# Kernel optimization log

Measured on AMD Instinct MI355X. Metric: run time of the kernel, lower is better.

Reference implementation:

```python
import jax, jax.numpy as jnp
import numpy as np

# --- constants mirroring init_kwargs ---
DIM = 1024
N_HEADS = 16
N_KV_HEADS = 4
HEAD_DIM = DIM // N_HEADS          # 64
REP = N_HEADS // N_KV_HEADS        # 4
ROPE_THETA = 10000.0
WINDOW = 512
N_GLOBAL = 64
EPS = 1e-6


def setup_inputs() -> dict:
    key = jax.random.key(0)
    ks = jax.random.split(key, 7)
    B, L = 2, 2048
    x = jax.random.normal(ks[0], (B, L, DIM), dtype=jnp.float32)
    s = 0.02
    wq = jax.random.normal(ks[1], (DIM, N_HEADS * HEAD_DIM), dtype=jnp.float32) * s
    wk = jax.random.normal(ks[2], (DIM, N_KV_HEADS * HEAD_DIM), dtype=jnp.float32) * s
    wv = jax.random.normal(ks[3], (DIM, N_KV_HEADS * HEAD_DIM), dtype=jnp.float32) * s
    wo = jax.random.normal(ks[4], (N_HEADS * HEAD_DIM, DIM), dtype=jnp.float32) * s
    gq = jnp.ones((HEAD_DIM,), dtype=jnp.float32) + 0.01 * jax.random.normal(ks[5], (HEAD_DIM,), dtype=jnp.float32)
    gk = jnp.ones((HEAD_DIM,), dtype=jnp.float32) + 0.01 * jax.random.normal(ks[6], (HEAD_DIM,), dtype=jnp.float32)
    return {"x": x, "wq": wq, "wk": wk, "wv": wv, "wo": wo, "gq": gq, "gk": gk}


def _rmsnorm(t, g):
    # QKNorm: RMS norm over head_dim with learnable per-dim scale
    return t * jax.lax.rsqrt(jnp.mean(t * t, axis=-1, keepdims=True) + EPS) * g


def _rope(t, cos, sin):
    # t: [B,H,L,hd]; complex RoPE over consecutive pairs (2i, 2i+1)
    t1 = t[..., 0::2]
    t2 = t[..., 1::2]
    o1 = t1 * cos - t2 * sin
    o2 = t1 * sin + t2 * cos
    return jnp.stack([o1, o2], axis=-1).reshape(t.shape)


def reference(x, wq, wk, wv, wo, gq, gk):
    B, L, D = x.shape
    q = (x @ wq).reshape(B, L, N_HEADS, HEAD_DIM)
    k = (x @ wk).reshape(B, L, N_KV_HEADS, HEAD_DIM)
    v = (x @ wv).reshape(B, L, N_KV_HEADS, HEAD_DIM)
    q = _rmsnorm(q, gq)
    k = _rmsnorm(k, gk)
    q = q.transpose(0, 2, 1, 3)  # [B,H,L,hd]
    k = k.transpose(0, 2, 1, 3)
    v = v.transpose(0, 2, 1, 3)

    # RoPE frequencies (start_pos = 0)
    inv_freq = 1.0 / (ROPE_THETA ** (jnp.arange(0, HEAD_DIM, 2, dtype=jnp.float32) / HEAD_DIM))
    ang = jnp.arange(L, dtype=jnp.float32)[:, None] * inv_freq[None, :]  # [L, hd/2]
    cos, sin = jnp.cos(ang), jnp.sin(ang)
    q = _rope(q, cos, sin)
    k = _rope(k, cos, sin)

    # GQA: repeat kv heads (repeat_interleave on head dim)
    k = jnp.repeat(k, REP, axis=1)
    v = jnp.repeat(v, REP, axis=1)

    scores = jnp.einsum("bhqd,bhkd->bhqk", q, k) / np.sqrt(HEAD_DIM).astype(np.float32)

    # sliding-window + global-token causal mask
    half = WINDOW // 2
    i = jnp.arange(L)[:, None]
    j = jnp.arange(L)[None, :]
    m = (j <= i) & ((j >= i - half) | (j < N_GLOBAL))  # [L,L] bool
    scores = jnp.where(m[None, None], scores, -jnp.inf)

    attn = jax.nn.softmax(scores.astype(jnp.float32), axis=-1).astype(scores.dtype)
    out = jnp.einsum("bhqk,bhkd->bhqd", attn, v)
    out = out.transpose(0, 2, 1, 3).reshape(B, L, N_HEADS * HEAD_DIM)
    return out @ wo
```

## Files before the change

### kernel.cpp

```cpp
#include <hip/hip_runtime.h>
#include <hip/hip_bf16.h>

typedef __bf16 bf16x8 __attribute__((ext_vector_type(8)));
typedef __bf16 bf16x4 __attribute__((ext_vector_type(4)));
typedef float  f32x4  __attribute__((ext_vector_type(4)));
typedef short  s16x4  __attribute__((ext_vector_type(4)));

__device__ __forceinline__ __bf16 to_bf16(float f) {
    __hip_bfloat16 h = __float2bfloat16(f);
    return *reinterpret_cast<__bf16*>(&h);
}

__device__ __forceinline__ f32x4 mfma32(bf16x8 a, bf16x8 b, f32x4 c) {
    return __builtin_amdgcn_mfma_f32_16x16x32_bf16(a, b, c, 0, 0, 0);
}
__device__ __forceinline__ f32x4 mfma16(bf16x4 a, bf16x4 b, f32x4 c) {
#if __has_builtin(__builtin_amdgcn_mfma_f32_16x16x16_bf16)
    return __builtin_amdgcn_mfma_f32_16x16x16_bf16(a, b, c, 0, 0, 0);
#else
    return __builtin_amdgcn_mfma_f32_16x16x16bf16_1k(
        __builtin_bit_cast(s16x4, a), __builtin_bit_cast(s16x4, b), c, 0, 0, 0);
#endif
}

__device__ __forceinline__ void gload_lds16(const __bf16* g, __bf16* l) {
    __builtin_amdgcn_global_load_lds(
        (const __attribute__((address_space(1))) void*)g,
        (__attribute__((address_space(3))) void*)l, 16, 0, 0);
}


__global__ __launch_bounds__(256) void prep_k(const float* __restrict__ wq,
                                              const float* __restrict__ wk,
                                              const float* __restrict__ wv,
                                              const float* __restrict__ wo,
                                              const float* __restrict__ x,
                                              __bf16* __restrict__ WqkvT,
                                              __bf16* __restrict__ WoT,
                                              __bf16* __restrict__ xb) {
    int b = blockIdx.x, tid = threadIdx.x;
    if (b >= 2560) {
        int i = ((b - 2560) * 256 + tid) * 8;
        f32x4 a = *(const f32x4*)(x + i);
        f32x4 c = *(const f32x4*)(x + i + 4);
        bf16x8 h;
        h[0] = to_bf16(a.x); h[1] = to_bf16(a.y); h[2] = to_bf16(a.z); h[3] = to_bf16(a.w);
        h[4] = to_bf16(c.x); h[5] = to_bf16(c.y); h[6] = to_bf16(c.z); h[7] = to_bf16(c.w);
        *(bf16x8*)(xb + i) = h;
        return;
    }
    __shared__ float tile[32][33];
    const float* src; __bf16* dst; int N, idx;
    if (b < 1024)      { src = wq; dst = WqkvT;                        N = 1024; idx = b; }
    else if (b < 1280) { src = wk; dst = WqkvT + (size_t)1024 * 1024;  N = 256;  idx = b - 1024; }
    else if (b < 1536) { src = wv; dst = WqkvT + (size_t)1280 * 1024;  N = 256;  idx = b - 1280; }
    else               { src = wo; dst = WoT;                          N = 1024; idx = b - 1536; }
    int k0 = (idx & 31) * 32, n0 = (idx >> 5) * 32;
    int tx = tid & 31, ty = tid >> 5;
#pragma unroll
    for (int r = 0; r < 4; ++r) {
        int kk = ty + r * 8;
        tile[kk][tx] = src[(size_t)(k0 + kk) * N + n0 + tx];
    }
    __syncthreads();
#pragma unroll
    for (int r = 0; r < 4; ++r) {
        int nn = ty + r * 8;
        dst[(size_t)(n0 + nn) * 1024 + k0 + tx] = to_bf16(tile[tx][nn]);
    }
}

__global__ __launch_bounds__(256) void gemmqkv_k(const __bf16* __restrict__ A,
                                                 const __bf16* __restrict__ BT,
                                                 const float* __restrict__ gq,
                                                 const float* __restrict__ gk,
                                                 __bf16* __restrict__ Qb,
                                                 __bf16* __restrict__ Kbl,
                                                 __bf16* __restrict__ Vt) {
    __shared__ __bf16 lA[128 * 32];
    __shared__ __bf16 lB[64 * 32];
    __shared__ float ssp[2][128];
    __shared__ __bf16 tv[64 * 136];
    const int K = 1024;
    int tid = threadIdx.x;
    int m0 = blockIdx.x * 128, n0 = blockIdx.y * 64;
    int head = n0 >> 6;
    int wid = tid >> 6, lane = tid & 63;
    int wm = (wid & 1) * 64, wn = (wid >> 1) * 32;
    int lm = lane & 15, qd = lane >> 4;

    f32x4 acc[4][2] = {};

    for (int k0 = 0; k0 < K; k0 += 32) {
#pragma unroll
        for (int it = 0; it < 2; ++it) {
            int c = it * 256 + tid;
            int row = c >> 2, c8 = c & 3;
            __bf16* la = lA + (it * 256 + wid * 64) * 8;
            gload_lds16(A + (size_t)(m0 + row) * K + k0 + c8 * 8, la);
        }
        {
            int row = tid >> 2, c8 = tid & 3;
            __bf16* lb = lB + (wid * 64) * 8;
            gload_lds16(BT + (size_t)(n0 + row) * K + k0 + c8 * 8, lb);
        }
        __syncthreads();

        bf16x8 af[4], bfr[2];
#pragma unroll
        for (int t = 0; t < 4; ++t)
            af[t] = *(const bf16x8*)&lA[(wm + t * 16 + lm) * 32 + qd * 8];
#pragma unroll
        for (int j = 0; j < 2; ++j)
            bfr[j] = *(const bf16x8*)&lB[(wn + j * 16 + lm) * 32 + qd * 8];
#pragma unroll
        for (int ti = 0; ti < 4; ++ti)
#pragma unroll
            for (int tj = 0; tj < 2; ++tj)
                acc[ti][tj] = mfma32(af[ti], bfr[tj], acc[ti][tj]);
        __syncthreads();
    }

    if (head < 20) {
#pragma unroll
        for (int ti = 0; ti < 4; ++ti)
#pragma unroll
            for (int r = 0; r < 4; ++r) {
                float sq = acc[ti][0][r] * acc[ti][0][r] + acc[ti][1][r] * acc[ti][1][r];
                sq += __shfl_xor(sq, 1);
                sq += __shfl_xor(sq, 2);
                sq += __shfl_xor(sq, 4);
                sq += __shfl_xor(sq, 8);
                if (lm == 0) ssp[wid >> 1][wm + ti * 16 + qd * 4 + r] = sq;
            }
        __syncthreads();

        bool isq = head < 16;
#pragma unroll
        for (int ti = 0; ti < 4; ++ti)
#pragma unroll
            for (int r = 0; r < 4; ++r) {
                int row = wm + ti * 16 + qd * 4 + r;
                int t = m0 + row;
                int pos = t & 2047, bb = t >> 11;
                float ss = ssp[0][row] + ssp[1][row];
                float scale = rsqrtf(ss * (1.0f / 64.0f) + 1e-6f);
#pragma unroll
                for (int tj = 0; tj < 2; ++tj) {
                    int col = wn + tj * 16 + lm;
                    float g = isq ? gq[col] : gk[col];
                    float v = acc[ti][tj][r] * scale * g;
                    float ex = (float)(2 * (col >> 1)) * (1.0f / 64.0f);
                    float invf = expf(-ex * 9.210340371976184f);
                    float ang = (float)pos * invf;
                    float c = cosf(ang), s = sinf(ang);
                    float pv = __shfl_xor(v, 1);
                    float outv = (col & 1) ? (pv * s + v * c) : (v * c - pv * s);
                    if (isq) {
                        int kvh = head >> 2, h4 = head & 3;
                        size_t off = (((((size_t)bb * 4 + kvh) * 128 + (pos >> 4)) * 4 + h4) * 16
                                      + (pos & 15)) * 64 + col;
                        Qb[off] = to_bf16(outv * 0.125f);
                    } else {
                        int kvg = head - 16;
                        Kbl[(((size_t)bb * 4 + kvg) * 2048 + pos) * 64 + col] = to_bf16(outv);
                    }
                }
            }
    } else {
#pragma unroll
        for (int ti = 0; ti < 4; ++ti)
#pragma unroll
            for (int tj = 0; tj < 2; ++tj)
#pragma unroll
                for (int r = 0; r < 4; ++r) {
                    int row = wm + ti * 16 + qd * 4 + r;
                    int col = wn + tj * 16 + lm;
                    tv[col * 136 + row] = to_bf16(acc[ti][tj][r]);
                }
        __syncthreads();
        int bb = m0 >> 11, kvg = head - 20;
        size_t gg = (size_t)bb * 4 + kvg;
        int pos0 = m0 & 2047;
#pragma unroll
        for (int p = 0; p < 4; ++p) {
            int d = p * 16 + (tid >> 4);
            int tok = (tid & 15) * 8;
            bf16x8 vvv = *(const bf16x8*)&tv[d * 136 + tok];
            *(bf16x8*)(Vt + (gg * 64 + d) * 2048 + pos0 + tok) = vvv;
        }
    }
}

__global__ __launch_bounds__(256) void gemm_bf16_k(const __bf16* __restrict__ A,
                                                   const __bf16* __restrict__ BT,
                                                   float* __restrict__ C,
                                                   int K, int N) {
    __shared__ __bf16 lA[128 * 32];
    __shared__ __bf16 lB[64 * 32];
    int tid = threadIdx.x;
    int m0 = blockIdx.x * 128, n0 = blockIdx.y * 64;
    int wid = tid >> 6, lane = tid & 63;
    int wm = (wid & 1) * 64, wn = (wid >> 1) * 32;
    int lm = lane & 15, qd = lane >> 4;

    f32x4 acc[4][2] = {};

    for (int k0 = 0; k0 < K; k0 += 32) {
#pragma unroll
        for (int it = 0; it < 2; ++it) {
            int c = it * 256 + tid;
            int row = c >> 2, c8 = c & 3;
            __bf16* la = lA + (it * 256 + wid * 64) * 8;
            gload_lds16(A + (size_t)(m0 + row) * K + k0 + c8 * 8, la);
        }
        {
            int row = tid >> 2, c8 = tid & 3;
            __bf16* lb = lB + (wid * 64) * 8;
            gload_lds16(BT + (size_t)(n0 + row) * K + k0 + c8 * 8, lb);
        }
        __syncthreads();

        bf16x8 af[4], bfr[2];
#pragma unroll
        for (int t = 0; t < 4; ++t)
            af[t] = *(const bf16x8*)&lA[(wm + t * 16 + lm) * 32 + qd * 8];
#pragma unroll
        for (int j = 0; j < 2; ++j)
            bfr[j] = *(const bf16x8*)&lB[(wn + j * 16 + lm) * 32 + qd * 8];
#pragma unroll
        for (int ti = 0; ti < 4; ++ti)
#pragma unroll
            for (int tj = 0; tj < 2; ++tj)
                acc[ti][tj] = mfma32(af[ti], bfr[tj], acc[ti][tj]);
        __syncthreads();
    }

#pragma unroll
    for (int ti = 0; ti < 4; ++ti)
#pragma unroll
        for (int tj = 0; tj < 2; ++tj)
#pragma unroll
            for (int r = 0; r < 4; ++r) {
                int row = m0 + wm + ti * 16 + qd * 4 + r;
                int col = n0 + wn + tj * 16 + lm;
                C[(size_t)row * N + col] = acc[ti][tj][r];
            }
}

__global__ __launch_bounds__(256) void attn_k(const __bf16* __restrict__ Qb,
                                              const __bf16* __restrict__ Kbl,
                                              const __bf16* __restrict__ Vt,
                                              __bf16* __restrict__ aout) {
    __shared__ __bf16 Kt[2][64 * 64];
    __shared__ __bf16 Vl[2][64 * 64];
    int tid = threadIdx.x, wid = tid >> 6, lane = tid & 63;
    int l15 = lane & 15, quad = lane >> 4;
    int qb = blockIdx.x, kvh = blockIdx.y, b = blockIdx.z;
    int iw = qb * 16;
    int g = b * 4 + kvh;
    int h = kvh * 4 + wid;
    int e7 = l15 & 7;

    const __bf16* qp = Qb + ((((size_t)g * 128 + qb) * 4 + wid) * 16 + l15) * 64 + quad * 8;
    bf16x8 qf0 = *(const bf16x8*)qp;
    bf16x8 qf1 = *(const bf16x8*)(qp + 32);

    int ts = (iw - 256) >> 6; if (ts < 1) ts = 1;
    int tmax = (iw + 15) >> 6;
    int n_all = (tmax >= ts) ? (tmax - ts + 2) : 1;

    const __bf16* Kg = Kbl + (size_t)g * 2048 * 64;
    const __bf16* Vg = Vt + (size_t)g * 64 * 2048;

    int r0 = tid >> 3, c0 = tid & 7;
    int kl0 = r0 * 64 + ((c0 ^ (r0 & 7)) * 8);
    int kl1 = kl0 + 32 * 64;

    bf16x8 kr0, kr1, vr0, vr1;
    auto stage_load = [&](int tt) {
        const __bf16* kb = Kg + (size_t)tt * 64 * 64;
        kr0 = *(const bf16x8*)(kb + r0 * 64 + c0 * 8);
        kr1 = *(const bf16x8*)(kb + (r0 + 32) * 64 + c0 * 8);
        const __bf16* vb = Vg + tt * 64 + c0 * 8;
        vr0 = *(const bf16x8*)(vb + (size_t)r0 * 2048);
        vr1 = *(const bf16x8*)(vb + (size_t)(r0 + 32) * 2048);
    };
    auto stage_write = [&](int buf) {
        *(bf16x8*)&Kt[buf][kl0] = kr0;
        *(bf16x8*)&Kt[buf][kl1] = kr1;
        *(bf16x8*)&Vl[buf][kl0] = vr0;
        *(bf16x8*)&Vl[buf][kl1] = vr1;
    };

    stage_load(0);
    stage_write(0);

    f32x4 o[4] = {};
    float mr = -1e30f, lrp = 0.f;
    int iq = iw + l15;

    for (int idx = 0; idx < n_all; ++idx) {
        int tt = (idx == 0) ? 0 : ts + idx - 1;
        if (idx + 1 < n_all) stage_load(ts + idx);
        __syncthreads();
        int buf = idx & 1;

        f32x4 s[4] = {};
#pragma unroll
        for (int nt = 0; nt < 4; ++nt) {
            const __bf16* kp = &Kt[buf][(nt * 16 + l15) * 64];
            bf16x8 k0 = *(const bf16x8*)(kp + ((quad ^ e7) * 8));
            bf16x8 k1 = *(const bf16x8*)(kp + (((quad + 4) ^ e7) * 8));
            s[nt] = mfma32(k0, qf0, s[nt]);
            s[nt] = mfma32(k1, qf1, s[nt]);
        }

        bool need_mask = (tt == tmax) || (tt >= 1 && tt * 64 < iw + 15 - 256);
        if (need_mask) {
#pragma unroll
            for (int nt = 0; nt < 4; ++nt)
#pragma unroll
                for (int r = 0; r < 4; ++r) {
                    int j = tt * 64 + nt * 16 + quad * 4 + r;
                    bool valid = (j <= iq) && ((j >= iq - 256) || (j < 64));
                    s[nt][r] = valid ? s[nt][r] : -1e30f;
                }
        }

        float mx = -1e30f;
#pragma unroll
        for (int nt = 0; nt < 4; ++nt)
#pragma unroll
            for (int r = 0; r < 4; ++r) mx = fmaxf(mx, s[nt][r]);
        mx = fmaxf(mx, __shfl_xor(mx, 16));
        mx = fmaxf(mx, __shfl_xor(mx, 32));
        float mn = fmaxf(mr, mx);
        float alpha = __expf(mr - mn);
        mr = mn;

        float ps = 0.f;
        bf16x4 pb[4];
#pragma unroll
        for (int nt = 0; nt < 4; ++nt)
#pragma unroll
            for (int r = 0; r < 4; ++r) {
                float pv = __expf(s[nt][r] - mn);
                ps += pv;
                pb[nt][r] = to_bf16(pv);
            }
        lrp = lrp * alpha + ps;

#pragma unroll
        for (int dt = 0; dt < 4; ++dt) {
            o[dt] *= alpha;
            const __bf16* vp = &Vl[buf][(dt * 16 + l15) * 64];
#pragma unroll
            for (int nt = 0; nt < 4; ++nt) {
                int c8 = 2 * nt + (quad >> 1);
                bf16x4 va = *(const bf16x4*)(vp + ((c8 ^ e7) * 8) + (quad & 1) * 4);
                o[dt] = mfma16(va, pb[nt], o[dt]);
            }
        }

        if (idx + 1 < n_all) stage_write((idx + 1) & 1);
    }

    lrp += __shfl_xor(lrp, 16);
    lrp += __shfl_xor(lrp, 32);
    float inv = 1.f / lrp;
    __syncthreads();
    __bf16* pr = &Kt[0][wid * 16 * 64];
#pragma unroll
    for (int dt = 0; dt < 4; ++dt)
#pragma unroll
        for (int r = 0; r < 4; ++r) {
            int e = dt * 16 + quad * 4 + r;
            int c8 = e >> 3;
            pr[l15 * 64 + ((c8 ^ e7) * 8) + (e & 7)] = to_bf16(o[dt][r] * inv);
        }
    bf16x8 o0 = *(const bf16x8*)(pr + l15 * 64 + (((2 * quad) ^ e7) * 8));
    bf16x8 o1 = *(const bf16x8*)(pr + l15 * 64 + (((2 * quad + 1) ^ e7) * 8));
    __bf16* op = aout + ((size_t)b * 2048 + iw + l15) * 1024 + h * 64 + quad * 16;
    *(bf16x8*)op = o0;
    *(bf16x8*)(op + 8) = o1;
}

extern "C" void kernel_launch(void* const* d_in, const int* in_sizes, int n_in,
                              void* d_out, int out_size, void* d_ws, size_t ws_size,
                              hipStream_t stream) {
    const float* x  = (const float*)d_in[0];
    const float* wq = (const float*)d_in[1];
    const float* wk = (const float*)d_in[2];
    const float* wv = (const float*)d_in[3];
    const float* wo = (const float*)d_in[4];
    const float* gq = (const float*)d_in[5];
    const float* gk = (const float*)d_in[6];
    float* out = (float*)d_out;

    char* ws = (char*)d_ws;
    __bf16* WqkvT = (__bf16*)ws;
    __bf16* WoT   = (__bf16*)(ws + 3145728);
    __bf16* xb_ao = (__bf16*)(ws + 5242880);
    __bf16* Kbl   = (__bf16*)(ws + 13631488);
    __bf16* Vt    = (__bf16*)(ws + 15728640);
    __bf16* Qb    = (__bf16*)(ws + 17825792);

    dim3 tb(256);
    prep_k<<<4608, tb, 0, stream>>>(wq, wk, wv, wo, x, WqkvT, WoT, xb_ao);
    gemmqkv_k<<<dim3(32, 24), tb, 0, stream>>>(xb_ao, WqkvT, gq, gk, Qb, Kbl, Vt);
    attn_k<<<dim3(128, 4, 2), tb, 0, stream>>>(Qb, Kbl, Vt, xb_ao);
    gemm_bf16_k<<<dim3(32, 16), tb, 0, stream>>>(xb_ao, WoT, out, 1024, 1024);
}
```

Measured before the change: 159.6 us.

## Deepen GEMM K-step to 64 and share K/V tiles across two query blocks

The shared GEMM core now loads a 64-wide K slab per iteration (two 32-wide halves), which halves the number of barriers and loop iterations in both projection GEMMs at the cost of doubled LDS tile size. The attention kernel moves to 512-thread blocks covering 32 queries (two 16-row groups times four heads), so each staged K/V tile is loaded once for twice as many queries, with one load per thread. The tile range now spans the union of both query groups, so some warps process extra masked tiles. Masking is extended to tt >= tmaxw to handle this, and the final output staging overlays both K buffers to fit eight warps.

```diff
diff --git a/kernel.cpp b/kernel.cpp
--- a/kernel.cpp
+++ b/kernel.cpp
@@ -70,6 +70,53 @@
     }
 }
 
+#define GEMM_CORE(A, BT, K)                                                     \
+    __shared__ __bf16 lA[8192];                                                 \
+    __shared__ __bf16 lB[4096];                                                 \
+    int tid = threadIdx.x;                                                      \
+    int m0 = blockIdx.x * 128, n0 = blockIdx.y * 64;                            \
+    int wid = tid >> 6, lane = tid & 63;                                        \
+    int wm = (wid & 1) * 64, wn = (wid >> 1) * 32;                              \
+    int lm = lane & 15, qd = lane >> 4;                                         \
+    f32x4 acc[4][2] = {};                                                       \
+    for (int k0 = 0; k0 < (K); k0 += 64) {                                      \
+        _Pragma("unroll")                                                       \
+        for (int it = 0; it < 4; ++it) {                                        \
+            int kh = it >> 1, half = it & 1;                                    \
+            int c = half * 256 + tid;                                           \
+            int row = c >> 2, c4 = c & 3;                                       \
+            __bf16* la = lA + kh * 4096 + half * 2048 + wid * 512;              \
+            gload_lds16((A) + (size_t)(m0 + row) * (K) + k0 + kh * 32 + c4 * 8, la); \
+        }                                                                       \
+        _Pragma("unroll")                                                       \
+        for (int kh = 0; kh < 2; ++kh) {                                        \
+            int row = tid >> 2, c4 = tid & 3;                                   \
+            __bf16* lb = lB + kh * 2048 + wid * 512;                            \
+            gload_lds16((BT) + (size_t)(n0 + row) * (K) + k0 + kh * 32 + c4 * 8, lb); \
+        }                                                                       \
+        __syncthreads();                                                        \
+        _Pragma("unroll")                                                       \
+        for (int kh = 0; kh < 2; ++kh) {                                        \
+            bf16x8 af[4], bfr[2];                                               \
+            _Pragma("unroll")                                                   \
+            for (int t = 0; t < 4; ++t) {                                       \
+                int row = wm + t * 16 + lm;                                     \
+                af[t] = *(const bf16x8*)&lA[kh * 4096 + (row >> 6) * 2048       \
+                                            + (row & 63) * 32 + qd * 8];        \
+            }                                                                   \
+            _Pragma("unroll")                                                   \
+            for (int j = 0; j < 2; ++j)                                         \
+                bfr[j] = *(const bf16x8*)&lB[kh * 2048 + (wn + j * 16 + lm) * 32 \
+                                             + qd * 8];                         \
+            _Pragma("unroll")                                                   \
+            for (int ti = 0; ti < 4; ++ti)                                      \
+                _Pragma("unroll")                                               \
+                for (int tj = 0; tj < 2; ++tj)                                  \
+                    acc[ti][tj] = mfma32(af[ti], bfr[tj], acc[ti][tj]);         \
+        }                                                                       \
+        __syncthreads();                                                        \
+    }
+
 __global__ __launch_bounds__(256) void gemmqkv_k(const __bf16* __restrict__ A,
                                                  const __bf16* __restrict__ BT,
                                                  const float* __restrict__ gq,
@@ -77,49 +124,10 @@
                                                  __bf16* __restrict__ Qb,
                                                  __bf16* __restrict__ Kbl,
                                                  __bf16* __restrict__ Vt) {
-    __shared__ __bf16 lA[128 * 32];
-    __shared__ __bf16 lB[64 * 32];
     __shared__ float ssp[2][128];
     __shared__ __bf16 tv[64 * 136];
-    const int K = 1024;
-    int tid = threadIdx.x;
-    int m0 = blockIdx.x * 128, n0 = blockIdx.y * 64;
+    GEMM_CORE(A, BT, 1024)
     int head = n0 >> 6;
-    int wid = tid >> 6, lane = tid & 63;
-    int wm = (wid & 1) * 64, wn = (wid >> 1) * 32;
-    int lm = lane & 15, qd = lane >> 4;
-
-    f32x4 acc[4][2] = {};
-
-    for (int k0 = 0; k0 < K; k0 += 32) {
-#pragma unroll
-        for (int it = 0; it < 2; ++it) {
-            int c = it * 256 + tid;
-            int row = c >> 2, c8 = c & 3;
-            __bf16* la = lA + (it * 256 + wid * 64) * 8;
-            gload_lds16(A + (size_t)(m0 + row) * K + k0 + c8 * 8, la);
-        }
-        {
-            int row = tid >> 2, c8 = tid & 3;
-            __bf16* lb = lB + (wid * 64) * 8;
-            gload_lds16(BT + (size_t)(n0 + row) * K + k0 + c8 * 8, lb);
-        }
-        __syncthreads();
-
-        bf16x8 af[4], bfr[2];
-#pragma unroll
-        for (int t = 0; t < 4; ++t)
-            af[t] = *(const bf16x8*)&lA[(wm + t * 16 + lm) * 32 + qd * 8];
-#pragma unroll
-        for (int j = 0; j < 2; ++j)
-            bfr[j] = *(const bf16x8*)&lB[(wn + j * 16 + lm) * 32 + qd * 8];
-#pragma unroll
-        for (int ti = 0; ti < 4; ++ti)
-#pragma unroll
-            for (int tj = 0; tj < 2; ++tj)
-                acc[ti][tj] = mfma32(af[ti], bfr[tj], acc[ti][tj]);
-        __syncthreads();
-    }
 
     if (head < 20) {
 #pragma unroll
@@ -196,46 +204,7 @@
                                                    const __bf16* __restrict__ BT,
                                                    float* __restrict__ C,
                                                    int K, int N) {
-    __shared__ __bf16 lA[128 * 32];
-    __shared__ __bf16 lB[64 * 32];
-    int tid = threadIdx.x;
-    int m0 = blockIdx.x * 128, n0 = blockIdx.y * 64;
-    int wid = tid >> 6, lane = tid & 63;
-    int wm = (wid & 1) * 64, wn = (wid >> 1) * 32;
-    int lm = lane & 15, qd = lane >> 4;
-
-    f32x4 acc[4][2] = {};
-
-    for (int k0 = 0; k0 < K; k0 += 32) {
-#pragma unroll
-        for (int it = 0; it < 2; ++it) {
-            int c = it * 256 + tid;
-            int row = c >> 2, c8 = c & 3;
-            __bf16* la = lA + (it * 256 + wid * 64) * 8;
-            gload_lds16(A + (size_t)(m0 + row) * K + k0 + c8 * 8, la);
-        }
-        {
-            int row = tid >> 2, c8 = tid & 3;
-            __bf16* lb = lB + (wid * 64) * 8;
-            gload_lds16(BT + (size_t)(n0 + row) * K + k0 + c8 * 8, lb);
-        }
-        __syncthreads();
-
-        bf16x8 af[4], bfr[2];
-#pragma unroll
-        for (int t = 0; t < 4; ++t)
-            af[t] = *(const bf16x8*)&lA[(wm + t * 16 + lm) * 32 + qd * 8];
-#pragma unroll
-        for (int j = 0; j < 2; ++j)
-            bfr[j] = *(const bf16x8*)&lB[(wn + j * 16 + lm) * 32 + qd * 8];
-#pragma unroll
-        for (int ti = 0; ti < 4; ++ti)
-#pragma unroll
-            for (int tj = 0; tj < 2; ++tj)
-                acc[ti][tj] = mfma32(af[ti], bfr[tj], acc[ti][tj]);
-        __syncthreads();
-    }
-
+    GEMM_CORE(A, BT, K)
 #pragma unroll
     for (int ti = 0; ti < 4; ++ti)
 #pragma unroll
@@ -248,7 +217,7 @@
             }
 }
 
-__global__ __launch_bounds__(256) void attn_k(const __bf16* __restrict__ Qb,
+__global__ __launch_bounds__(512) void attn_k(const __bf16* __restrict__ Qb,
                                               const __bf16* __restrict__ Kbl,
                                               const __bf16* __restrict__ Vt,
                                               __bf16* __restrict__ aout) {
@@ -257,40 +226,38 @@
     int tid = threadIdx.x, wid = tid >> 6, lane = tid & 63;
     int l15 = lane & 15, quad = lane >> 4;
     int qb = blockIdx.x, kvh = blockIdx.y, b = blockIdx.z;
-    int iw = qb * 16;
+    int qg = wid >> 2;
+    int h4 = wid & 3;
+    int iw0 = qb * 32;
+    int iw = iw0 + qg * 16;
     int g = b * 4 + kvh;
-    int h = kvh * 4 + wid;
+    int h = kvh * 4 + h4;
     int e7 = l15 & 7;
 
-    const __bf16* qp = Qb + ((((size_t)g * 128 + qb) * 4 + wid) * 16 + l15) * 64 + quad * 8;
+    int qbi = qb * 2 + qg;
+    const __bf16* qp = Qb + ((((size_t)g * 128 + qbi) * 4 + h4) * 16 + l15) * 64 + quad * 8;
     bf16x8 qf0 = *(const bf16x8*)qp;
     bf16x8 qf1 = *(const bf16x8*)(qp + 32);
 
-    int ts = (iw - 256) >> 6; if (ts < 1) ts = 1;
-    int tmax = (iw + 15) >> 6;
-    int n_all = (tmax >= ts) ? (tmax - ts + 2) : 1;
+    int ts = (iw0 - 256) >> 6; if (ts < 1) ts = 1;
+    int tmaxb = (iw0 + 31) >> 6;
+    int n_all = (tmaxb >= ts) ? (tmaxb - ts + 2) : 1;
+    int tmaxw = (iw + 15) >> 6;
 
     const __bf16* Kg = Kbl + (size_t)g * 2048 * 64;
     const __bf16* Vg = Vt + (size_t)g * 64 * 2048;
 
     int r0 = tid >> 3, c0 = tid & 7;
-    int kl0 = r0 * 64 + ((c0 ^ (r0 & 7)) * 8);
-    int kl1 = kl0 + 32 * 64;
-
-    bf16x8 kr0, kr1, vr0, vr1;
+    int kl = r0 * 64 + ((c0 ^ (r0 & 7)) * 8);
+
+    bf16x8 kr, vr;
     auto stage_load = [&](int tt) {
-        const __bf16* kb = Kg + (size_t)tt * 64 * 64;
-        kr0 = *(const bf16x8*)(kb + r0 * 64 + c0 * 8);
-        kr1 = *(const bf16x8*)(kb + (r0 + 32) * 64 + c0 * 8);
-        const __bf16* vb = Vg + tt * 64 + c0 * 8;
-        vr0 = *(const bf16x8*)(vb + (size_t)r0 * 2048);
-        vr1 = *(const bf16x8*)(vb + (size_t)(r0 + 32) * 2048);
+        kr = *(const bf16x8*)(Kg + (size_t)tt * 64 * 64 + r0 * 64 + c0 * 8);
+        vr = *(const bf16x8*)(Vg + (size_t)r0 * 2048 + tt * 64 + c0 * 8);
     };
     auto stage_write = [&](int buf) {
-        *(bf16x8*)&Kt[buf][kl0] = kr0;
-        *(bf16x8*)&Kt[buf][kl1] = kr1;
-        *(bf16x8*)&Vl[buf][kl0] = vr0;
-        *(bf16x8*)&Vl[buf][kl1] = vr1;
+        *(bf16x8*)&Kt[buf][kl] = kr;
+        *(bf16x8*)&Vl[buf][kl] = vr;
     };
 
     stage_load(0);
@@ -316,7 +283,7 @@
             s[nt] = mfma32(k1, qf1, s[nt]);
         }
 
-        bool need_mask = (tt == tmax) || (tt >= 1 && tt * 64 < iw + 15 - 256);
+        bool need_mask = (tt >= tmaxw) || (tt >= 1 && tt * 64 < iw + 15 - 256);
         if (need_mask) {
 #pragma unroll
             for (int nt = 0; nt < 4; ++nt)
@@ -370,7 +337,7 @@
     lrp += __shfl_xor(lrp, 32);
     float inv = 1.f / lrp;
     __syncthreads();
-    __bf16* pr = &Kt[0][wid * 16 * 64];
+    __bf16* pr = (__bf16*)Kt + wid * 16 * 64;
 #pragma unroll
     for (int dt = 0; dt < 4; ++dt)
 #pragma unroll
@@ -409,6 +376,6 @@
     dim3 tb(256);
     prep_k<<<4608, tb, 0, stream>>>(wq, wk, wv, wo, x, WqkvT, WoT, xb_ao);
     gemmqkv_k<<<dim3(32, 24), tb, 0, stream>>>(xb_ao, WqkvT, gq, gk, Qb, Kbl, Vt);
-    attn_k<<<dim3(128, 4, 2), tb, 0, stream>>>(Qb, Kbl, Vt, xb_ao);
+    attn_k<<<dim3(64, 4, 2), dim3(512), 0, stream>>>(Qb, Kbl, Vt, xb_ao);
     gemm_bf16_k<<<dim3(32, 16), tb, 0, stream>>>(xb_ao, WoT, out, 1024, 1024);
 }
```

New measurement: 149.2 us. 1.07x faster.
